# Kernel tuning notes

Hardware: AMD Instinct MI355X
Metric: run time of the kernel (lower is better)

The kernel has to match this reference:

```python
import jax, jax.numpy as jnp
import numpy as np

N_NODES = 100000
N_EDGES = 1600000


def setup_inputs() -> dict:
    key = jax.random.key(0)
    k1, k2, k3, k4 = jax.random.split(key, 4)
    x = jax.random.normal(k1, (N_NODES, 16), dtype=jnp.float32)
    edge_index = jax.random.randint(k2, (2, N_EDGES), 0, N_NODES, dtype=jnp.int32)
    # Glorot-ish init for the two GCN layers
    W1 = jax.random.normal(k3, (16, 32), dtype=jnp.float32) * (1.0 / np.sqrt(16))
    b1 = jnp.zeros((32,), dtype=jnp.float32)
    W2 = jax.random.normal(k4, (32, 2), dtype=jnp.float32) * (1.0 / np.sqrt(32))
    b2 = jnp.zeros((2,), dtype=jnp.float32)
    return {"x": x, "edge_index": edge_index, "W1": W1, "b1": b1, "W2": W2, "b2": b2}


def _gcn_conv(x, W, b, src, dst, norm, n_nodes):
    # PyG GCNConv: h = X @ W; aggregate norm * h[src] at dst; add bias.
    h = x @ W                                   # [N, out]
    msg = h[src] * norm[:, None]                # [E+N, out] gather + scale
    out = jax.ops.segment_sum(msg, dst, num_segments=n_nodes)
    return out + b


def reference(x, edge_index, W1, b1, W2, b2):
    n = x.shape[0]
    self_loops = jnp.arange(n, dtype=edge_index.dtype)
    src = jnp.concatenate([edge_index[0], self_loops])  # [E+N]
    dst = jnp.concatenate([edge_index[1], self_loops])
    # Symmetric GCN normalization: deg computed on graph with self-loops
    deg = jax.ops.segment_sum(jnp.ones_like(dst, dtype=x.dtype), dst, num_segments=n)
    dis = jnp.where(deg > 0, jax.lax.rsqrt(deg), 0.0)   # deg^{-1/2}
    norm = dis[src] * dis[dst]                          # [E+N]

    h = jax.nn.relu(_gcn_conv(x, W1, b1, src, dst, norm, n))
    out = _gcn_conv(h, W2, b2, src, dst, norm, n)
    return out
```

## Files before the change

### kernel.cpp

```cpp
#include <hip/hip_runtime.h>
#include <hip/hip_fp16.h>

static constexpr int N  = 100000;
static constexpr int E  = 1600000;
static constexpr int B  = 256;

static constexpr int BC     = 1024;
static constexpr int NBLKC  = 256;
static constexpr int CHUNKC = E / NBLKC;
static constexpr int PERC   = (CHUNKC + BC - 1) / BC;
static constexpr int NBUCK  = (N + 127) / 128;
static constexpr int SLAB   = 3072;
static constexpr int GCS    = 16;


__global__ __launch_bounds__(BC) void kC_scatter(
        const int* __restrict__ src, const int* __restrict__ dst,
        int* __restrict__ gcur, int* __restrict__ gslab) {
    __shared__ int lhist[NBUCK];
    __shared__ int lbase[NBUCK];
    __shared__ int gb[NBUCK];
    __shared__ int wsum[16];
    __shared__ int stage[CHUNKC];

    int t = threadIdx.x, blk = blockIdx.x;
    for (int i = t; i < NBUCK; i += BC) lhist[i] = 0;
    __syncthreads();

    int eb = blk * CHUNKC;
    int ds[PERC], ss[PERC];
#pragma unroll
    for (int k = 0; k < PERC; ++k) {
        int idx = k * BC + t;
        if (idx < CHUNKC) {
            ds[k] = dst[eb + idx];
            ss[k] = src[eb + idx];
            atomicAdd(&lhist[ds[k] >> 7], 1);
        }
    }
    __syncthreads();

    int lane = t & 63, wv = t >> 6;
    int val = (t < NBUCK) ? lhist[t] : 0;
    int inc = val;
#pragma unroll
    for (int off = 1; off < 64; off <<= 1) {
        int u = __shfl_up(inc, off, 64);
        if (lane >= off) inc += u;
    }
    if (lane == 63) wsum[wv] = inc;
    __syncthreads();
    if (wv == 0) {
        int wval = (lane < 16) ? wsum[lane] : 0;
        int winc = wval;
#pragma unroll
        for (int off = 1; off < 16; off <<= 1) {
            int u = __shfl_up(winc, off, 64);
            if (lane >= off) winc += u;
        }
        if (lane < 16) wsum[lane] = winc - wval;
    }
    __syncthreads();
    if (t < NBUCK) lbase[t] = wsum[wv] + inc - val;
    __syncthreads();

    if (t < NBUCK) {
        int h = lhist[t];
        if (h > 0) gb[t] = t * SLAB + atomicAdd(&gcur[t * GCS], h);
        lhist[t] = 0;
    }
    __syncthreads();

#pragma unroll
    for (int k = 0; k < PERC; ++k) {
        int idx = k * BC + t;
        if (idx < CHUNKC) {
            int d = ds[k], b = d >> 7;
            int r = atomicAdd(&lhist[b], 1);
            stage[lbase[b] + r] = ss[k] | ((d & 127) << 17);
        }
    }
    __syncthreads();

    if (t < NBUCK) {
        int len = lhist[t];
        if (len > 0) {
            int s0 = lbase[t];
            int g  = gb[t];
            int cap = (t + 1) * SLAB - g;
            if (cap < 0) cap = 0;
            if (len > cap) len = cap;
            for (int i = 0; i < len; ++i) gslab[g + i] = stage[s0 + i];
        }
    }
}


__global__ void kD1_deg(const int* __restrict__ gcur, const int* __restrict__ gslab,
                        int* __restrict__ rofs, const float4* __restrict__ x4,
                        __half* __restrict__ xpre) {
    __shared__ int c[128];
    __shared__ int wq[2];
    int t = threadIdx.x, b = blockIdx.x;
    if (t < 128) c[t] = 0;
    __syncthreads();

    int ne = min(gcur[b * GCS], SLAB);
    int base = b * SLAB;
    int ne4 = ne & ~3;
    for (int k = 4 * t; k < ne4; k += 4 * B) {
        int4 p4 = *(const int4*)(gslab + base + k);
        atomicAdd(&c[p4.x >> 17], 1);
        atomicAdd(&c[p4.y >> 17], 1);
        atomicAdd(&c[p4.z >> 17], 1);
        atomicAdd(&c[p4.w >> 17], 1);
    }
    if (t < ne - ne4) atomicAdd(&c[gslab[base + ne4 + t] >> 17], 1);
    __syncthreads();

    int lane = t & 63, wv = t >> 6;
    int val = (t < 128) ? c[t] : 0;
    int inc = val;
#pragma unroll
    for (int off = 1; off < 64; off <<= 1) {
        int u = __shfl_up(inc, off, 64);
        if (lane >= off) inc += u;
    }
    if (t == 63) wq[0] = inc;
    __syncthreads();
    if (t < 128) rofs[b * 129 + t] = base + inc - val + ((wv == 1) ? wq[0] : 0);
    if (t == 128) rofs[b * 129 + 128] = base + ne;

    int n = b * 128 + (t >> 1), h = t & 1;
    if (n < N) {
        float d = rsqrtf((float)(c[t >> 1] + 1));
        float4 u0 = x4[(size_t)n * 4 + h * 2];
        float4 u1 = x4[(size_t)n * 4 + h * 2 + 1];
        ushort4 p0, p1;
        p0.x = __half_as_ushort(__float2half(u0.x * d));
        p0.y = __half_as_ushort(__float2half(u0.y * d));
        p0.z = __half_as_ushort(__float2half(u0.z * d));
        p0.w = __half_as_ushort(__float2half(u0.w * d));
        p1.x = __half_as_ushort(__float2half(u1.x * d));
        p1.y = __half_as_ushort(__float2half(u1.y * d));
        p1.z = __half_as_ushort(__float2half(u1.z * d));
        p1.w = __half_as_ushort(__float2half(u1.w * d));
        *(ushort4*)(xpre + (size_t)n * 16 + h * 8)     = p0;
        *(ushort4*)(xpre + (size_t)n * 16 + h * 8 + 4) = p1;
    }
}


__global__ __launch_bounds__(B) void kD2_agg(
        const __half* __restrict__ xpre, int* __restrict__ gslab,
        const int* __restrict__ rofs, const float* __restrict__ W1,
        const float* __restrict__ b1, const float* __restrict__ W2,
        float2* __restrict__ hpre) {
    __shared__ int st1[SLAB];
    __shared__ int cur[128];
    __shared__ int lofs[129];
    __shared__ float acc[128 * 17];
    __shared__ float sW1[512], sb1[32], sW2[64];
    int t = threadIdx.x, b = blockIdx.x;
    for (int i = t; i < 512; i += B) sW1[i] = W1[i];
    if (t < 32) sb1[t] = b1[t];
    if (t < 64) sW2[t] = W2[t];
    if (t < 128) cur[t] = 0;
    int base = b * SLAB;
    if (t < 129) lofs[t] = rofs[b * 129 + t] - base;
    __syncthreads();

    int ne = lofs[128];
    for (int k = t; k < ne; k += B) {
        int p = gslab[base + k];
        int lo = p >> 17;
        int r = atomicAdd(&cur[lo], 1);
        st1[lofs[lo] + r] = p & 0x1FFFF;
    }
    __syncthreads();
    for (int k = t; k < ne; k += B) gslab[base + k] = st1[k];

    int nl = t >> 1, h = t & 1;
    int n = b * 128 + nl;
    if (n < N) {
        int rs = lofs[nl], re = lofs[nl + 1];
        float a0, a1, a2, a3, a4, a5, a6, a7;
        {
            int4 w = *(const int4*)(xpre + (size_t)n * 16 + h * 8);
            float2 q0 = __half22float2(*(__half2*)&w.x);
            float2 q1 = __half22float2(*(__half2*)&w.y);
            float2 q2 = __half22float2(*(__half2*)&w.z);
            float2 q3 = __half22float2(*(__half2*)&w.w);
            a0 = q0.x; a1 = q0.y; a2 = q1.x; a3 = q1.y;
            a4 = q2.x; a5 = q2.y; a6 = q3.x; a7 = q3.y;
        }
        auto add8 = [&](int4 w) {
            float2 q0 = __half22float2(*(__half2*)&w.x);
            float2 q1 = __half22float2(*(__half2*)&w.y);
            float2 q2 = __half22float2(*(__half2*)&w.z);
            float2 q3 = __half22float2(*(__half2*)&w.w);
            a0 += q0.x; a1 += q0.y; a2 += q1.x; a3 += q1.y;
            a4 += q2.x; a5 += q2.y; a6 += q3.x; a7 += q3.y;
        };
        int k = rs;
        for (; k + 4 <= re; k += 4) {
            int s0 = st1[k], s1 = st1[k + 1], s2 = st1[k + 2], s3 = st1[k + 3];
            int4 v0 = *(const int4*)(xpre + (size_t)s0 * 16 + h * 8);
            int4 v1 = *(const int4*)(xpre + (size_t)s1 * 16 + h * 8);
            int4 v2 = *(const int4*)(xpre + (size_t)s2 * 16 + h * 8);
            int4 v3 = *(const int4*)(xpre + (size_t)s3 * 16 + h * 8);
            add8(v0); add8(v1); add8(v2); add8(v3);
        }
        for (; k < re; ++k)
            add8(*(const int4*)(xpre + (size_t)st1[k] * 16 + h * 8));
        float* row = acc + nl * 17 + h * 8;
        row[0] = a0; row[1] = a1; row[2] = a2; row[3] = a3;
        row[4] = a4; row[5] = a5; row[6] = a6; row[7] = a7;
    }
    __syncthreads();

    if (t < 128) {
        int n2 = b * 128 + t;
        if (n2 < N) {
            int deg = lofs[t + 1] - lofs[t];
            float d = rsqrtf((float)(deg + 1));
            const float* row = acc + t * 17;
            float xi[16];
#pragma unroll
            for (int k = 0; k < 16; ++k) xi[k] = row[k] * d;
            float o0 = 0.f, o1 = 0.f;
#pragma unroll
            for (int c = 0; c < 32; ++c) {
                float hh = sb1[c];
#pragma unroll
                for (int k = 0; k < 16; ++k) hh = fmaf(xi[k], sW1[k * 32 + c], hh);
                hh = fmaxf(hh, 0.f);
                o0 = fmaf(hh, sW2[c * 2 + 0], o0);
                o1 = fmaf(hh, sW2[c * 2 + 1], o1);
            }
            hpre[n2] = make_float2(d * o0, d * o1);
        }
    }
}


__global__ void kF_l2(const float2* __restrict__ hpre, const int* __restrict__ gslab,
                      const int* __restrict__ rofs, const float* __restrict__ b2,
                      float2* __restrict__ out) {
    int n = blockIdx.x * B + threadIdx.x;
    if (n >= N) return;
    int bb = n >> 7, lo = n & 127;
    int rs = rofs[bb * 129 + lo], re = rofs[bb * 129 + lo + 1];
    float2 self = hpre[n];
    float o0 = self.x, o1 = self.y;
    int k = rs;
    for (; k + 4 <= re; k += 4) {
        int s0 = gslab[k], s1 = gslab[k + 1], s2 = gslab[k + 2], s3 = gslab[k + 3];
        float2 v0 = hpre[s0];
        float2 v1 = hpre[s1];
        float2 v2 = hpre[s2];
        float2 v3 = hpre[s3];
        o0 += (v0.x + v1.x) + (v2.x + v3.x);
        o1 += (v0.y + v1.y) + (v2.y + v3.y);
    }
    for (; k < re; ++k) {
        float2 v = hpre[gslab[k]];
        o0 += v.x; o1 += v.y;
    }
    float d = rsqrtf((float)(re - rs + 1));
    out[n] = make_float2(fmaf(d, o0, b2[0]), fmaf(d, o1, b2[1]));
}


extern "C" void kernel_launch(void* const* d_in, const int* in_sizes, int n_in,
                              void* d_out, int out_size, void* d_ws, size_t ws_size,
                              hipStream_t stream) {
    const float* x  = (const float*)d_in[0];
    const int*   ei = (const int*)d_in[1];
    const float* W1 = (const float*)d_in[2];
    const float* b1 = (const float*)d_in[3];
    const float* W2 = (const float*)d_in[4];
    const float* b2 = (const float*)d_in[5];

    const int* src = ei;
    const int* dst = ei + E;

    int*    gslab = (int*)d_ws;
    int*    rofs  = gslab + (size_t)NBUCK * SLAB;
    int*    gcur  = rofs + 100880;
    float*  hpre  = (float*)(gcur + 12512);
    __half* xpre  = (__half*)(hpre + 2 * (size_t)N);

    hipMemsetAsync(gcur, 0, NBUCK * GCS * sizeof(int), stream);
    kC_scatter<<<NBLKC, BC, 0, stream>>>(src, dst, gcur, gslab);
    kD1_deg<<<NBUCK, B, 0, stream>>>(gcur, gslab, rofs, (const float4*)x, xpre);
    kD2_agg<<<NBUCK, B, 0, stream>>>(xpre, gslab, rofs, W1, b1, W2, (float2*)hpre);
    kF_l2<<<(N + B - 1) / B, B, 0, stream>>>((const float2*)hpre, gslab, rofs, b2,
                                             (float2*)d_out);
}
```

Measured before the change: 128.8 us.

## Fuse degree, layer-1 and layer-2 kernels into one persistent kernel with grid barriers

```diff
diff --git a/kernel.cpp b/kernel.cpp
--- a/kernel.cpp
+++ b/kernel.cpp
@@ -12,6 +12,7 @@
 static constexpr int NBUCK  = (N + 127) / 128;
 static constexpr int SLAB   = 3072;
 static constexpr int GCS    = 16;
+static constexpr int BF     = 256;
 
 
 __global__ __launch_bounds__(BC) void kC_scatter(
@@ -96,19 +97,48 @@
 }
 
 
-__global__ void kD1_deg(const int* __restrict__ gcur, const int* __restrict__ gslab,
-                        int* __restrict__ rofs, const float4* __restrict__ x4,
-                        __half* __restrict__ xpre) {
-    __shared__ int c[128];
-    __shared__ int wq[2];
+__device__ __forceinline__ void grid_barrier(int* bar, int slot) {
+    __syncthreads();
+    __threadfence();
+    if (threadIdx.x == 0) {
+        __hip_atomic_fetch_add(&bar[slot * 16], 1, __ATOMIC_ACQ_REL,
+                               __HIP_MEMORY_SCOPE_AGENT);
+        long budget = 1L << 27;
+        while (__hip_atomic_load(&bar[slot * 16], __ATOMIC_ACQUIRE,
+                                 __HIP_MEMORY_SCOPE_AGENT) < NBUCK &&
+               --budget > 0) {}
+    }
+    __syncthreads();
+}
+
+
+__global__ __launch_bounds__(BF) void kFused(
+        const int* __restrict__ gcur, const int* __restrict__ gslab,
+        const float4* __restrict__ x4, __half* __restrict__ xpre,
+        const float* __restrict__ W1, const float* __restrict__ b1,
+        const float* __restrict__ W2, const float* __restrict__ b2,
+        float2* __restrict__ hpre, float2* __restrict__ out,
+        int* __restrict__ bar) {
+    __shared__ int st1[SLAB];
+    __shared__ int c[128], cur[128];
+    __shared__ int lofs[129];
+    __shared__ float acc[128 * 17];
+    __shared__ float sW1[512], sb1[32], sW2[64];
+    __shared__ int wq;
+
     int t = threadIdx.x, b = blockIdx.x;
-    if (t < 128) c[t] = 0;
+    int base = b * SLAB;
+    int nbase = b * 128;
+
+    if (t < 32) sb1[t] = b1[t];
+    if (t < 64) sW2[t] = W2[t];
+    sW1[t] = W1[t]; sW1[t + 256] = W1[t + 256];
+    if (t < 128) { c[t] = 0; cur[t] = 0; }
     __syncthreads();
 
     int ne = min(gcur[b * GCS], SLAB);
-    int base = b * SLAB;
     int ne4 = ne & ~3;
-    for (int k = 4 * t; k < ne4; k += 4 * B) {
+    for (int k = 4 * t; k < ne4; k += 4 * BF) {
         int4 p4 = *(const int4*)(gslab + base + k);
         atomicAdd(&c[p4.x >> 17], 1);
         atomicAdd(&c[p4.y >> 17], 1);
@@ -118,109 +148,93 @@
     if (t < ne - ne4) atomicAdd(&c[gslab[base + ne4 + t] >> 17], 1);
     __syncthreads();
 
-    int lane = t & 63, wv = t >> 6;
-    int val = (t < 128) ? c[t] : 0;
-    int inc = val;
-#pragma unroll
-    for (int off = 1; off < 64; off <<= 1) {
-        int u = __shfl_up(inc, off, 64);
-        if (lane >= off) inc += u;
-    }
-    if (t == 63) wq[0] = inc;
-    __syncthreads();
-    if (t < 128) rofs[b * 129 + t] = base + inc - val + ((wv == 1) ? wq[0] : 0);
-    if (t == 128) rofs[b * 129 + 128] = base + ne;
-
-    int n = b * 128 + (t >> 1), h = t & 1;
-    if (n < N) {
-        float d = rsqrtf((float)(c[t >> 1] + 1));
-        float4 u0 = x4[(size_t)n * 4 + h * 2];
-        float4 u1 = x4[(size_t)n * 4 + h * 2 + 1];
-        ushort4 p0, p1;
-        p0.x = __half_as_ushort(__float2half(u0.x * d));
-        p0.y = __half_as_ushort(__float2half(u0.y * d));
-        p0.z = __half_as_ushort(__float2half(u0.z * d));
-        p0.w = __half_as_ushort(__float2half(u0.w * d));
-        p1.x = __half_as_ushort(__float2half(u1.x * d));
-        p1.y = __half_as_ushort(__float2half(u1.y * d));
-        p1.z = __half_as_ushort(__float2half(u1.z * d));
-        p1.w = __half_as_ushort(__float2half(u1.w * d));
-        *(ushort4*)(xpre + (size_t)n * 16 + h * 8)     = p0;
-        *(ushort4*)(xpre + (size_t)n * 16 + h * 8 + 4) = p1;
-    }
-}
-
-
-__global__ __launch_bounds__(B) void kD2_agg(
-        const __half* __restrict__ xpre, int* __restrict__ gslab,
-        const int* __restrict__ rofs, const float* __restrict__ W1,
-        const float* __restrict__ b1, const float* __restrict__ W2,
-        float2* __restrict__ hpre) {
-    __shared__ int st1[SLAB];
-    __shared__ int cur[128];
-    __shared__ int lofs[129];
-    __shared__ float acc[128 * 17];
-    __shared__ float sW1[512], sb1[32], sW2[64];
-    int t = threadIdx.x, b = blockIdx.x;
-    for (int i = t; i < 512; i += B) sW1[i] = W1[i];
-    if (t < 32) sb1[t] = b1[t];
-    if (t < 64) sW2[t] = W2[t];
-    if (t < 128) cur[t] = 0;
-    int base = b * SLAB;
-    if (t < 129) lofs[t] = rofs[b * 129 + t] - base;
-    __syncthreads();
-
-    int ne = lofs[128];
-    for (int k = t; k < ne; k += B) {
+    {
+        int lane = t & 63, wv = t >> 6;
+        int val = (t < 128) ? c[t] : 0;
+        int inc = val;
+#pragma unroll
+        for (int off = 1; off < 64; off <<= 1) {
+            int u = __shfl_up(inc, off, 64);
+            if (lane >= off) inc += u;
+        }
+        if (t == 63) wq = inc;
+        __syncthreads();
+        if (t < 128) lofs[t] = inc - val + ((wv == 1) ? wq : 0);
+        if (t == 128) lofs[128] = ne;
+    }
+
+    {
+        int n = nbase + (t >> 1), h = t & 1;
+        if (n < N) {
+            float d = rsqrtf((float)(c[t >> 1] + 1));
+            float4 u0 = x4[(size_t)n * 4 + h * 2];
+            float4 u1 = x4[(size_t)n * 4 + h * 2 + 1];
+            ushort4 p0, p1;
+            p0.x = __half_as_ushort(__float2half(u0.x * d));
+            p0.y = __half_as_ushort(__float2half(u0.y * d));
+            p0.z = __half_as_ushort(__float2half(u0.z * d));
+            p0.w = __half_as_ushort(__float2half(u0.w * d));
+            p1.x = __half_as_ushort(__float2half(u1.x * d));
+            p1.y = __half_as_ushort(__float2half(u1.y * d));
+            p1.z = __half_as_ushort(__float2half(u1.z * d));
+            p1.w = __half_as_ushort(__float2half(u1.w * d));
+            *(ushort4*)(xpre + (size_t)n * 16 + h * 8)     = p0;
+            *(ushort4*)(xpre + (size_t)n * 16 + h * 8 + 4) = p1;
+        }
+    }
+    grid_barrier(bar, 0);
+
+    for (int k = t; k < ne; k += BF) {
         int p = gslab[base + k];
         int lo = p >> 17;
         int r = atomicAdd(&cur[lo], 1);
         st1[lofs[lo] + r] = p & 0x1FFFF;
     }
     __syncthreads();
-    for (int k = t; k < ne; k += B) gslab[base + k] = st1[k];
-
-    int nl = t >> 1, h = t & 1;
-    int n = b * 128 + nl;
-    if (n < N) {
-        int rs = lofs[nl], re = lofs[nl + 1];
-        float a0, a1, a2, a3, a4, a5, a6, a7;
-        {
-            int4 w = *(const int4*)(xpre + (size_t)n * 16 + h * 8);
-            float2 q0 = __half22float2(*(__half2*)&w.x);
-            float2 q1 = __half22float2(*(__half2*)&w.y);
-            float2 q2 = __half22float2(*(__half2*)&w.z);
-            float2 q3 = __half22float2(*(__half2*)&w.w);
-            a0 = q0.x; a1 = q0.y; a2 = q1.x; a3 = q1.y;
-            a4 = q2.x; a5 = q2.y; a6 = q3.x; a7 = q3.y;
-        }
-        auto add8 = [&](int4 w) {
-            float2 q0 = __half22float2(*(__half2*)&w.x);
-            float2 q1 = __half22float2(*(__half2*)&w.y);
-            float2 q2 = __half22float2(*(__half2*)&w.z);
-            float2 q3 = __half22float2(*(__half2*)&w.w);
-            a0 += q0.x; a1 += q0.y; a2 += q1.x; a3 += q1.y;
-            a4 += q2.x; a5 += q2.y; a6 += q3.x; a7 += q3.y;
-        };
-        int k = rs;
-        for (; k + 4 <= re; k += 4) {
-            int s0 = st1[k], s1 = st1[k + 1], s2 = st1[k + 2], s3 = st1[k + 3];
-            int4 v0 = *(const int4*)(xpre + (size_t)s0 * 16 + h * 8);
-            int4 v1 = *(const int4*)(xpre + (size_t)s1 * 16 + h * 8);
-            int4 v2 = *(const int4*)(xpre + (size_t)s2 * 16 + h * 8);
-            int4 v3 = *(const int4*)(xpre + (size_t)s3 * 16 + h * 8);
-            add8(v0); add8(v1); add8(v2); add8(v3);
-        }
-        for (; k < re; ++k)
-            add8(*(const int4*)(xpre + (size_t)st1[k] * 16 + h * 8));
-        float* row = acc + nl * 17 + h * 8;
-        row[0] = a0; row[1] = a1; row[2] = a2; row[3] = a3;
-        row[4] = a4; row[5] = a5; row[6] = a6; row[7] = a7;
+
+    {
+        int nl = t >> 1, h = t & 1;
+        int n = nbase + nl;
+        if (n < N) {
+            int rs = lofs[nl], re = lofs[nl + 1];
+            float a0, a1, a2, a3, a4, a5, a6, a7;
+            {
+                int4 w = *(const int4*)(xpre + (size_t)n * 16 + h * 8);
+                float2 q0 = __half22float2(*(__half2*)&w.x);
+                float2 q1 = __half22float2(*(__half2*)&w.y);
+                float2 q2 = __half22float2(*(__half2*)&w.z);
+                float2 q3 = __half22float2(*(__half2*)&w.w);
+                a0 = q0.x; a1 = q0.y; a2 = q1.x; a3 = q1.y;
+                a4 = q2.x; a5 = q2.y; a6 = q3.x; a7 = q3.y;
+            }
+            auto add8 = [&](int4 w) {
+                float2 q0 = __half22float2(*(__half2*)&w.x);
+                float2 q1 = __half22float2(*(__half2*)&w.y);
+                float2 q2 = __half22float2(*(__half2*)&w.z);
+                float2 q3 = __half22float2(*(__half2*)&w.w);
+                a0 += q0.x; a1 += q0.y; a2 += q1.x; a3 += q1.y;
+                a4 += q2.x; a5 += q2.y; a6 += q3.x; a7 += q3.y;
+            };
+            int k = rs;
+            for (; k + 4 <= re; k += 4) {
+                int s0 = st1[k], s1 = st1[k + 1], s2 = st1[k + 2], s3 = st1[k + 3];
+                int4 v0 = *(const int4*)(xpre + (size_t)s0 * 16 + h * 8);
+                int4 v1 = *(const int4*)(xpre + (size_t)s1 * 16 + h * 8);
+                int4 v2 = *(const int4*)(xpre + (size_t)s2 * 16 + h * 8);
+                int4 v3 = *(const int4*)(xpre + (size_t)s3 * 16 + h * 8);
+                add8(v0); add8(v1); add8(v2); add8(v3);
+            }
+            for (; k < re; ++k)
+                add8(*(const int4*)(xpre + (size_t)st1[k] * 16 + h * 8));
+            float* row = acc + nl * 17 + h * 8;
+            row[0] = a0; row[1] = a1; row[2] = a2; row[3] = a3;
+            row[4] = a4; row[5] = a5; row[6] = a6; row[7] = a7;
+        }
     }
     __syncthreads();
 
     if (t < 128) {
-        int n2 = b * 128 + t;
+        int n2 = nbase + t;
         if (n2 < N) {
             int deg = lofs[t + 1] - lofs[t];
             float d = rsqrtf((float)(deg + 1));
@@ -230,45 +244,52 @@
             for (int k = 0; k < 16; ++k) xi[k] = row[k] * d;
             float o0 = 0.f, o1 = 0.f;
 #pragma unroll
-            for (int c = 0; c < 32; ++c) {
-                float hh = sb1[c];
-#pragma unroll
-                for (int k = 0; k < 16; ++k) hh = fmaf(xi[k], sW1[k * 32 + c], hh);
+            for (int cc = 0; cc < 32; ++cc) {
+                float hh = sb1[cc];
+#pragma unroll
+                for (int k = 0; k < 16; ++k) hh = fmaf(xi[k], sW1[k * 32 + cc], hh);
                 hh = fmaxf(hh, 0.f);
-                o0 = fmaf(hh, sW2[c * 2 + 0], o0);
-                o1 = fmaf(hh, sW2[c * 2 + 1], o1);
+                o0 = fmaf(hh, sW2[cc * 2 + 0], o0);
+                o1 = fmaf(hh, sW2[cc * 2 + 1], o1);
             }
             hpre[n2] = make_float2(d * o0, d * o1);
         }
     }
-}
-
-
-__global__ void kF_l2(const float2* __restrict__ hpre, const int* __restrict__ gslab,
-                      const int* __restrict__ rofs, const float* __restrict__ b2,
-                      float2* __restrict__ out) {
-    int n = blockIdx.x * B + threadIdx.x;
-    if (n >= N) return;
-    int bb = n >> 7, lo = n & 127;
-    int rs = rofs[bb * 129 + lo], re = rofs[bb * 129 + lo + 1];
-    float2 self = hpre[n];
-    float o0 = self.x, o1 = self.y;
-    int k = rs;
-    for (; k + 4 <= re; k += 4) {
-        int s0 = gslab[k], s1 = gslab[k + 1], s2 = gslab[k + 2], s3 = gslab[k + 3];
-        float2 v0 = hpre[s0];
-        float2 v1 = hpre[s1];
-        float2 v2 = hpre[s2];
-        float2 v3 = hpre[s3];
-        o0 += (v0.x + v1.x) + (v2.x + v3.x);
-        o1 += (v0.y + v1.y) + (v2.y + v3.y);
-    }
-    for (; k < re; ++k) {
-        float2 v = hpre[gslab[k]];
-        o0 += v.x; o1 += v.y;
-    }
-    float d = rsqrtf((float)(re - rs + 1));
-    out[n] = make_float2(fmaf(d, o0, b2[0]), fmaf(d, o1, b2[1]));
+    grid_barrier(bar, 1);
+
+    {
+        int nl = t >> 1, eh = t & 1;
+        int n = nbase + nl;
+        float o0 = 0.f, o1 = 0.f;
+        int rs = 0, re = 0;
+        if (n < N) {
+            rs = lofs[nl]; re = lofs[nl + 1];
+            if (eh == 0) {
+                float2 self = hpre[n];
+                o0 = self.x; o1 = self.y;
+            }
+            int k = rs + eh;
+            for (; k + 6 < re; k += 8) {
+                int s0 = st1[k], s1 = st1[k + 2], s2 = st1[k + 4], s3 = st1[k + 6];
+                float2 v0 = hpre[s0];
+                float2 v1 = hpre[s1];
+                float2 v2 = hpre[s2];
+                float2 v3 = hpre[s3];
+                o0 += (v0.x + v1.x) + (v2.x + v3.x);
+                o1 += (v0.y + v1.y) + (v2.y + v3.y);
+            }
+            for (; k < re; k += 2) {
+                float2 v = hpre[st1[k]];
+                o0 += v.x; o1 += v.y;
+            }
+        }
+        o0 += __shfl_xor(o0, 1, 64);
+        o1 += __shfl_xor(o1, 1, 64);
+        if (n < N && eh == 0) {
+            float d = rsqrtf((float)(re - rs + 1));
+            out[n] = make_float2(fmaf(d, o0, b2[0]), fmaf(d, o1, b2[1]));
+        }
+    }
 }
 
 
@@ -286,15 +307,15 @@
     const int* dst = ei + E;
 
     int*    gslab = (int*)d_ws;
-    int*    rofs  = gslab + (size_t)NBUCK * SLAB;
-    int*    gcur  = rofs + 100880;
-    float*  hpre  = (float*)(gcur + 12512);
+    int*    gcur  = gslab + (size_t)NBUCK * SLAB;
+    int*    bar   = gcur + 12512;
+    float*  hpre  = (float*)(bar + 48);
     __half* xpre  = (__half*)(hpre + 2 * (size_t)N);
 
-    hipMemsetAsync(gcur, 0, NBUCK * GCS * sizeof(int), stream);
+    hipMemsetAsync(gcur, 0, (12512 + 48) * sizeof(int), stream);
     kC_scatter<<<NBLKC, BC, 0, stream>>>(src, dst, gcur, gslab);
-    kD1_deg<<<NBUCK, B, 0, stream>>>(gcur, gslab, rofs, (const float4*)x, xpre);
-    kD2_agg<<<NBUCK, B, 0, stream>>>(xpre, gslab, rofs, W1, b1, W2, (float2*)hpre);
-    kF_l2<<<(N + B - 1) / B, B, 0, stream>>>((const float2*)hpre, gslab, rofs, b2,
-                                             (float2*)d_out);
+
+    kFused<<<NBUCK, BF, 0, stream>>>(gcur, gslab, (const float4*)x, xpre,
+                                     W1, b1, W2, b2,
+                                     (float2*)hpre, (float2*)d_out, bar);
 }
```

Result: slower. 331.2 us (+157.2%).

## Halve bucket size to 64 nodes and split edge gather across four threads per node

Applied to the files above, without the earlier changes.

```diff
diff --git a/kernel.cpp b/kernel.cpp
--- a/kernel.cpp
+++ b/kernel.cpp
@@ -9,8 +9,8 @@
 static constexpr int NBLKC  = 256;
 static constexpr int CHUNKC = E / NBLKC;
 static constexpr int PERC   = (CHUNKC + BC - 1) / BC;
-static constexpr int NBUCK  = (N + 127) / 128;
-static constexpr int SLAB   = 3072;
+static constexpr int NBUCK  = (N + 63) / 64;
+static constexpr int SLAB   = 1536;
 static constexpr int GCS    = 16;
 
 
@@ -35,14 +35,17 @@
         if (idx < CHUNKC) {
             ds[k] = dst[eb + idx];
             ss[k] = src[eb + idx];
-            atomicAdd(&lhist[ds[k] >> 7], 1);
+            atomicAdd(&lhist[ds[k] >> 6], 1);
         }
     }
     __syncthreads();
 
     int lane = t & 63, wv = t >> 6;
-    int val = (t < NBUCK) ? lhist[t] : 0;
-    int inc = val;
+    int i0 = 2 * t;
+    int v0 = (i0 < NBUCK) ? lhist[i0] : 0;
+    int v1 = (i0 + 1 < NBUCK) ? lhist[i0 + 1] : 0;
+    int sum = v0 + v1;
+    int inc = sum;
 #pragma unroll
     for (int off = 1; off < 64; off <<= 1) {
         int u = __shfl_up(inc, off, 64);
@@ -61,13 +64,17 @@
         if (lane < 16) wsum[lane] = winc - wval;
     }
     __syncthreads();
-    if (t < NBUCK) lbase[t] = wsum[wv] + inc - val;
-    __syncthreads();
-
-    if (t < NBUCK) {
-        int h = lhist[t];
-        if (h > 0) gb[t] = t * SLAB + atomicAdd(&gcur[t * GCS], h);
-        lhist[t] = 0;
+    {
+        int ex = wsum[wv] + inc - sum;
+        if (i0 < NBUCK) lbase[i0] = ex;
+        if (i0 + 1 < NBUCK) lbase[i0 + 1] = ex + v0;
+    }
+    __syncthreads();
+
+    for (int bb = t; bb < NBUCK; bb += BC) {
+        int h = lhist[bb];
+        if (h > 0) gb[bb] = bb * SLAB + atomicAdd(&gcur[bb * GCS], h);
+        lhist[bb] = 0;
     }
     __syncthreads();
 
@@ -75,19 +82,19 @@
     for (int k = 0; k < PERC; ++k) {
         int idx = k * BC + t;
         if (idx < CHUNKC) {
-            int d = ds[k], b = d >> 7;
+            int d = ds[k], b = d >> 6;
             int r = atomicAdd(&lhist[b], 1);
-            stage[lbase[b] + r] = ss[k] | ((d & 127) << 17);
-        }
-    }
-    __syncthreads();
-
-    if (t < NBUCK) {
-        int len = lhist[t];
+            stage[lbase[b] + r] = ss[k] | ((d & 63) << 17);
+        }
+    }
+    __syncthreads();
+
+    for (int bb = t; bb < NBUCK; bb += BC) {
+        int len = lhist[bb];
         if (len > 0) {
-            int s0 = lbase[t];
-            int g  = gb[t];
-            int cap = (t + 1) * SLAB - g;
+            int s0 = lbase[bb];
+            int g  = gb[bb];
+            int cap = (bb + 1) * SLAB - g;
             if (cap < 0) cap = 0;
             if (len > cap) len = cap;
             for (int i = 0; i < len; ++i) gslab[g + i] = stage[s0 + i];
@@ -99,10 +106,9 @@
 __global__ void kD1_deg(const int* __restrict__ gcur, const int* __restrict__ gslab,
                         int* __restrict__ rofs, const float4* __restrict__ x4,
                         __half* __restrict__ xpre) {
-    __shared__ int c[128];
-    __shared__ int wq[2];
+    __shared__ int c[64];
     int t = threadIdx.x, b = blockIdx.x;
-    if (t < 128) c[t] = 0;
+    if (t < 64) c[t] = 0;
     __syncthreads();
 
     int ne = min(gcur[b * GCS], SLAB);
@@ -118,21 +124,19 @@
     if (t < ne - ne4) atomicAdd(&c[gslab[base + ne4 + t] >> 17], 1);
     __syncthreads();
 
-    int lane = t & 63, wv = t >> 6;
-    int val = (t < 128) ? c[t] : 0;
+    int lane = t & 63;
+    int val = (t < 64) ? c[t] : 0;
     int inc = val;
 #pragma unroll
     for (int off = 1; off < 64; off <<= 1) {
         int u = __shfl_up(inc, off, 64);
         if (lane >= off) inc += u;
     }
-    if (t == 63) wq[0] = inc;
-    __syncthreads();
-    if (t < 128) rofs[b * 129 + t] = base + inc - val + ((wv == 1) ? wq[0] : 0);
-    if (t == 128) rofs[b * 129 + 128] = base + ne;
-
-    int n = b * 128 + (t >> 1), h = t & 1;
-    if (n < N) {
+    if (t < 64) rofs[b * 65 + t] = base + inc - val;
+    if (t == 64) rofs[b * 65 + 64] = base + ne;
+
+    int n = b * 64 + (t >> 1), h = t & 1;
+    if (t < 128 && n < N) {
         float d = rsqrtf((float)(c[t >> 1] + 1));
         float4 u0 = x4[(size_t)n * 4 + h * 2];
         float4 u1 = x4[(size_t)n * 4 + h * 2 + 1];
@@ -157,20 +161,20 @@
         const float* __restrict__ b1, const float* __restrict__ W2,
         float2* __restrict__ hpre) {
     __shared__ int st1[SLAB];
-    __shared__ int cur[128];
-    __shared__ int lofs[129];
-    __shared__ float acc[128 * 17];
+    __shared__ int cur[64];
+    __shared__ int lofs[65];
+    __shared__ float acc[64 * 17];
     __shared__ float sW1[512], sb1[32], sW2[64];
     int t = threadIdx.x, b = blockIdx.x;
     for (int i = t; i < 512; i += B) sW1[i] = W1[i];
     if (t < 32) sb1[t] = b1[t];
     if (t < 64) sW2[t] = W2[t];
-    if (t < 128) cur[t] = 0;
+    if (t < 64) cur[t] = 0;
     int base = b * SLAB;
-    if (t < 129) lofs[t] = rofs[b * 129 + t] - base;
-    __syncthreads();
-
-    int ne = lofs[128];
+    if (t < 65) lofs[t] = rofs[b * 65 + t] - base;
+    __syncthreads();
+
+    int ne = lofs[64];
     for (int k = t; k < ne; k += B) {
         int p = gslab[base + k];
         int lo = p >> 17;
@@ -180,47 +184,56 @@
     __syncthreads();
     for (int k = t; k < ne; k += B) gslab[base + k] = st1[k];
 
-    int nl = t >> 1, h = t & 1;
-    int n = b * 128 + nl;
-    if (n < N) {
-        int rs = lofs[nl], re = lofs[nl + 1];
-        float a0, a1, a2, a3, a4, a5, a6, a7;
-        {
-            int4 w = *(const int4*)(xpre + (size_t)n * 16 + h * 8);
-            float2 q0 = __half22float2(*(__half2*)&w.x);
-            float2 q1 = __half22float2(*(__half2*)&w.y);
-            float2 q2 = __half22float2(*(__half2*)&w.z);
-            float2 q3 = __half22float2(*(__half2*)&w.w);
-            a0 = q0.x; a1 = q0.y; a2 = q1.x; a3 = q1.y;
-            a4 = q2.x; a5 = q2.y; a6 = q3.x; a7 = q3.y;
-        }
-        auto add8 = [&](int4 w) {
-            float2 q0 = __half22float2(*(__half2*)&w.x);
-            float2 q1 = __half22float2(*(__half2*)&w.y);
-            float2 q2 = __half22float2(*(__half2*)&w.z);
-            float2 q3 = __half22float2(*(__half2*)&w.w);
-            a0 += q0.x; a1 += q0.y; a2 += q1.x; a3 += q1.y;
-            a4 += q2.x; a5 += q2.y; a6 += q3.x; a7 += q3.y;
-        };
-        int k = rs;
-        for (; k + 4 <= re; k += 4) {
-            int s0 = st1[k], s1 = st1[k + 1], s2 = st1[k + 2], s3 = st1[k + 3];
-            int4 v0 = *(const int4*)(xpre + (size_t)s0 * 16 + h * 8);
-            int4 v1 = *(const int4*)(xpre + (size_t)s1 * 16 + h * 8);
-            int4 v2 = *(const int4*)(xpre + (size_t)s2 * 16 + h * 8);
-            int4 v3 = *(const int4*)(xpre + (size_t)s3 * 16 + h * 8);
-            add8(v0); add8(v1); add8(v2); add8(v3);
-        }
-        for (; k < re; ++k)
-            add8(*(const int4*)(xpre + (size_t)st1[k] * 16 + h * 8));
-        float* row = acc + nl * 17 + h * 8;
-        row[0] = a0; row[1] = a1; row[2] = a2; row[3] = a3;
-        row[4] = a4; row[5] = a5; row[6] = a6; row[7] = a7;
-    }
-    __syncthreads();
-
-    if (t < 128) {
-        int n2 = b * 128 + t;
+    {
+        int nl = t >> 2, h = t & 1, eh = (t >> 1) & 1;
+        int n = b * 64 + nl;
+        float a0 = 0.f, a1 = 0.f, a2 = 0.f, a3 = 0.f;
+        float a4 = 0.f, a5 = 0.f, a6 = 0.f, a7 = 0.f;
+        if (n < N) {
+            int rs = lofs[nl], re = lofs[nl + 1];
+            if (eh == 0) {
+                int4 w = *(const int4*)(xpre + (size_t)n * 16 + h * 8);
+                float2 q0 = __half22float2(*(__half2*)&w.x);
+                float2 q1 = __half22float2(*(__half2*)&w.y);
+                float2 q2 = __half22float2(*(__half2*)&w.z);
+                float2 q3 = __half22float2(*(__half2*)&w.w);
+                a0 = q0.x; a1 = q0.y; a2 = q1.x; a3 = q1.y;
+                a4 = q2.x; a5 = q2.y; a6 = q3.x; a7 = q3.y;
+            }
+            auto add8 = [&](int4 w) {
+                float2 q0 = __half22float2(*(__half2*)&w.x);
+                float2 q1 = __half22float2(*(__half2*)&w.y);
+                float2 q2 = __half22float2(*(__half2*)&w.z);
+                float2 q3 = __half22float2(*(__half2*)&w.w);
+                a0 += q0.x; a1 += q0.y; a2 += q1.x; a3 += q1.y;
+                a4 += q2.x; a5 += q2.y; a6 += q3.x; a7 += q3.y;
+            };
+            int k = rs + eh;
+            for (; k + 6 < re; k += 8) {
+                int s0 = st1[k], s1 = st1[k + 2], s2 = st1[k + 4], s3 = st1[k + 6];
+                int4 v0 = *(const int4*)(xpre + (size_t)s0 * 16 + h * 8);
+                int4 v1 = *(const int4*)(xpre + (size_t)s1 * 16 + h * 8);
+                int4 v2 = *(const int4*)(xpre + (size_t)s2 * 16 + h * 8);
+                int4 v3 = *(const int4*)(xpre + (size_t)s3 * 16 + h * 8);
+                add8(v0); add8(v1); add8(v2); add8(v3);
+            }
+            for (; k < re; k += 2)
+                add8(*(const int4*)(xpre + (size_t)st1[k] * 16 + h * 8));
+        }
+        a0 += __shfl_xor(a0, 2, 64); a1 += __shfl_xor(a1, 2, 64);
+        a2 += __shfl_xor(a2, 2, 64); a3 += __shfl_xor(a3, 2, 64);
+        a4 += __shfl_xor(a4, 2, 64); a5 += __shfl_xor(a5, 2, 64);
+        a6 += __shfl_xor(a6, 2, 64); a7 += __shfl_xor(a7, 2, 64);
+        if (n < N && eh == 0) {
+            float* row = acc + nl * 17 + h * 8;
+            row[0] = a0; row[1] = a1; row[2] = a2; row[3] = a3;
+            row[4] = a4; row[5] = a5; row[6] = a6; row[7] = a7;
+        }
+    }
+    __syncthreads();
+
+    if (t < 64) {
+        int n2 = b * 64 + t;
         if (n2 < N) {
             int deg = lofs[t + 1] - lofs[t];
             float d = rsqrtf((float)(deg + 1));
@@ -249,8 +262,8 @@
                       float2* __restrict__ out) {
     int n = blockIdx.x * B + threadIdx.x;
     if (n >= N) return;
-    int bb = n >> 7, lo = n & 127;
-    int rs = rofs[bb * 129 + lo], re = rofs[bb * 129 + lo + 1];
+    int bb = n >> 6, lo = n & 63;
+    int rs = rofs[bb * 65 + lo], re = rofs[bb * 65 + lo + 1];
     float2 self = hpre[n];
     float o0 = self.x, o1 = self.y;
     int k = rs;
@@ -287,8 +300,8 @@
 
     int*    gslab = (int*)d_ws;
     int*    rofs  = gslab + (size_t)NBUCK * SLAB;
-    int*    gcur  = rofs + 100880;
-    float*  hpre  = (float*)(gcur + 12512);
+    int*    gcur  = rofs + 101600;
+    float*  hpre  = (float*)(gcur + 25008);
     __half* xpre  = (__half*)(hpre + 2 * (size_t)N);
 
     hipMemsetAsync(gcur, 0, NBUCK * GCS * sizeof(int), stream);
```

Measured after the change: 138.2 us. 7.3% more time.

## Drop sorted-slab writeback and re-sort bucket in LDS inside layer-2 kernel

Applied to the files above, without the earlier changes.

```diff
diff --git a/kernel.cpp b/kernel.cpp
--- a/kernel.cpp
+++ b/kernel.cpp
@@ -152,7 +152,7 @@
 
 
 __global__ __launch_bounds__(B) void kD2_agg(
-        const __half* __restrict__ xpre, int* __restrict__ gslab,
+        const __half* __restrict__ xpre, const int* __restrict__ gslab,
         const int* __restrict__ rofs, const float* __restrict__ W1,
         const float* __restrict__ b1, const float* __restrict__ W2,
         float2* __restrict__ hpre) {
@@ -178,7 +178,6 @@
         st1[lofs[lo] + r] = p & 0x1FFFF;
     }
     __syncthreads();
-    for (int k = t; k < ne; k += B) gslab[base + k] = st1[k];
 
     int nl = t >> 1, h = t & 1;
     int n = b * 128 + nl;
@@ -244,31 +243,59 @@
 }
 
 
-__global__ void kF_l2(const float2* __restrict__ hpre, const int* __restrict__ gslab,
-                      const int* __restrict__ rofs, const float* __restrict__ b2,
-                      float2* __restrict__ out) {
-    int n = blockIdx.x * B + threadIdx.x;
-    if (n >= N) return;
-    int bb = n >> 7, lo = n & 127;
-    int rs = rofs[bb * 129 + lo], re = rofs[bb * 129 + lo + 1];
-    float2 self = hpre[n];
-    float o0 = self.x, o1 = self.y;
-    int k = rs;
-    for (; k + 4 <= re; k += 4) {
-        int s0 = gslab[k], s1 = gslab[k + 1], s2 = gslab[k + 2], s3 = gslab[k + 3];
-        float2 v0 = hpre[s0];
-        float2 v1 = hpre[s1];
-        float2 v2 = hpre[s2];
-        float2 v3 = hpre[s3];
-        o0 += (v0.x + v1.x) + (v2.x + v3.x);
-        o1 += (v0.y + v1.y) + (v2.y + v3.y);
-    }
-    for (; k < re; ++k) {
-        float2 v = hpre[gslab[k]];
-        o0 += v.x; o1 += v.y;
-    }
-    float d = rsqrtf((float)(re - rs + 1));
-    out[n] = make_float2(fmaf(d, o0, b2[0]), fmaf(d, o1, b2[1]));
+__global__ __launch_bounds__(B) void kF_l2(
+        const float2* __restrict__ hpre, const int* __restrict__ gslab,
+        const int* __restrict__ rofs, const float* __restrict__ b2,
+        float2* __restrict__ out) {
+    __shared__ int st1[SLAB];
+    __shared__ int cur[128];
+    __shared__ int lofs[129];
+    int t = threadIdx.x, b = blockIdx.x;
+    if (t < 128) cur[t] = 0;
+    int base = b * SLAB;
+    if (t < 129) lofs[t] = rofs[b * 129 + t] - base;
+    __syncthreads();
+
+    int ne = lofs[128];
+    for (int k = t; k < ne; k += B) {
+        int p = gslab[base + k];
+        int lo = p >> 17;
+        int r = atomicAdd(&cur[lo], 1);
+        st1[lofs[lo] + r] = p & 0x1FFFF;
+    }
+    __syncthreads();
+
+    int nl = t >> 1, eh = t & 1;
+    int n = b * 128 + nl;
+    float o0 = 0.f, o1 = 0.f;
+    int rs = 0, re = 0;
+    if (n < N) {
+        rs = lofs[nl]; re = lofs[nl + 1];
+        if (eh == 0) {
+            float2 self = hpre[n];
+            o0 = self.x; o1 = self.y;
+        }
+        int k = rs + eh;
+        for (; k + 6 < re; k += 8) {
+            int s0 = st1[k], s1 = st1[k + 2], s2 = st1[k + 4], s3 = st1[k + 6];
+            float2 v0 = hpre[s0];
+            float2 v1 = hpre[s1];
+            float2 v2 = hpre[s2];
+            float2 v3 = hpre[s3];
+            o0 += (v0.x + v1.x) + (v2.x + v3.x);
+            o1 += (v0.y + v1.y) + (v2.y + v3.y);
+        }
+        for (; k < re; k += 2) {
+            float2 v = hpre[st1[k]];
+            o0 += v.x; o1 += v.y;
+        }
+    }
+    o0 += __shfl_xor(o0, 1, 64);
+    o1 += __shfl_xor(o1, 1, 64);
+    if (n < N && eh == 0) {
+        float d = rsqrtf((float)(re - rs + 1));
+        out[n] = make_float2(fmaf(d, o0, b2[0]), fmaf(d, o1, b2[1]));
+    }
 }
 
 
@@ -295,6 +322,6 @@
     kC_scatter<<<NBLKC, BC, 0, stream>>>(src, dst, gcur, gslab);
     kD1_deg<<<NBUCK, B, 0, stream>>>(gcur, gslab, rofs, (const float4*)x, xpre);
     kD2_agg<<<NBUCK, B, 0, stream>>>(xpre, gslab, rofs, W1, b1, W2, (float2*)hpre);
-    kF_l2<<<(N + B - 1) / B, B, 0, stream>>>((const float2*)hpre, gslab, rofs, b2,
-                                             (float2*)d_out);
-}
+    kF_l2<<<NBUCK, B, 0, stream>>>((const float2*)hpre, gslab, rofs, b2,
+                                   (float2*)d_out);
+}
```

Result: no change. 126.8 us (median of 2 runs) (-1.5%).
